# Kernel optimization log

Measured on AMD Instinct MI355X. Metric: run time of the kernel, lower is better.

The kernel has to match this reference:

```python
import jax, jax.numpy as jnp
import numpy as np

N, E, D, T, B, OUT = 20000, 80000, 768, 4, 3, 768
SCALE = 0.02


def _layer_norm(x, g, b):
    mu = jnp.mean(x, axis=-1, keepdims=True)
    var = jnp.var(x, axis=-1, keepdims=True)
    return (x - mu) / jnp.sqrt(var + 1e-5) * g + b


def _typed_linear(x, etype, bases, coeff):
    # DGL TypedLinear with basis regularizer: W[t] = sum_b coeff[t,b] * bases[b]
    # computed as 3 shared GEMMs + per-edge weighted sum (avoids [E,D,D] gather).
    c = coeff[etype]  # [E, B]
    y = c[:, 0:1] * (x @ bases[0])
    for bb in range(1, bases.shape[0]):
        y = y + c[:, bb:bb + 1] * (x @ bases[bb])
    return y


def _time_encode(t, freq, phase):
    return jnp.cos(t[:, None] * freq[None, :] + phase[None, :])


def _segment_softmax(scores, seg, n):
    m = jax.ops.segment_max(scores, seg, num_segments=n)
    m = jnp.where(jnp.isfinite(m), m, 0.0)  # empty segments -> -inf guard
    e = jnp.exp(scores - m[seg])
    den = jax.ops.segment_sum(e, seg, num_segments=n)[seg]
    return e / jnp.where(den == 0, 1.0, den)


def _forward(h, etime_hete, first_etime_homo, second_etime_homo, w_src, w_dst,
             ln_g, ln_b, src_bases, src_coeff, dst_bases, dst_coeff,
             user_bases, user_coeff, lin_w, lin_b, time_freq, time_phase,
             src_hete, dst_hete, first_etype_hete, src_homo, dst_homo,
             first_etype_homo, second_etype_homo, n_nodes):
    inv_sqrt_d = 1.0 / jnp.sqrt(jnp.asarray(768.0, h.dtype))
    n_src = h @ w_src.T  # src_weight (no bias)
    n_dst = h @ w_dst.T  # dst_weight (no bias)

    # --- heterogeneous edges ---
    sf = n_src[src_hete]
    df = n_dst[dst_hete]
    hete_src = jax.nn.relu(_typed_linear(_layer_norm(sf, ln_g, ln_b), first_etype_hete, src_bases, src_coeff))
    msg_h = _time_encode(etime_hete, time_freq, time_phase) + hete_src
    e_h = jnp.sum(msg_h * df, axis=1) * inv_sqrt_d
    a_h = _segment_softmax(e_h, dst_hete, n_nodes)
    h_hete = jax.ops.segment_sum(a_h[:, None] * msg_h, dst_hete, num_segments=n_nodes)

    # --- homogeneous edges ---
    sf = n_src[src_homo]
    df = n_dst[dst_homo]
    dst_feat = jax.nn.relu(_typed_linear(_layer_norm(df, ln_g, ln_b), first_etype_homo, dst_bases, dst_coeff))
    homo_feat = jax.nn.relu(_typed_linear(_layer_norm(sf, ln_g, ln_b), second_etype_homo, user_bases, user_coeff))
    t_homo = jnp.maximum(first_etime_homo, second_etime_homo)
    msg_o = _time_encode(t_homo, time_freq, time_phase) + homo_feat
    e_o = jnp.sum(msg_o * dst_feat, axis=1) * inv_sqrt_d
    a_o = _segment_softmax(e_o, dst_homo, n_nodes)
    h_homo = jax.ops.segment_sum(a_o[:, None] * msg_o, dst_homo, num_segments=n_nodes)

    n = jnp.concatenate([h_hete, h_homo], axis=-1)  # [N, 2D]
    z = jax.nn.relu(n @ lin_w.T + lin_b)
    zn = jnp.linalg.norm(z, axis=1, keepdims=True)
    return z / jnp.where(zn == 0, 1.0, zn)


def setup_inputs() -> dict:
    key = jax.random.key(0)
    ks = jax.random.split(key, 24)
    inp = {
        'h': jax.random.normal(ks[0], (N, D), jnp.float32),
        'etime_hete': jax.random.uniform(ks[1], (E,), jnp.float32),
        'first_etime_homo': jax.random.uniform(ks[2], (E,), jnp.float32),
        'second_etime_homo': jax.random.uniform(ks[3], (E,), jnp.float32),
        'w_src': jax.random.normal(ks[4], (D, D), jnp.float32) * SCALE,
        'w_dst': jax.random.normal(ks[5], (D, D), jnp.float32) * SCALE,
        'ln_g': jnp.ones((D,), jnp.float32),
        'ln_b': jnp.zeros((D,), jnp.float32),
        'src_bases': jax.random.normal(ks[6], (B, D, D), jnp.float32) * SCALE,
        'src_coeff': jax.random.normal(ks[7], (T, B), jnp.float32),
        'dst_bases': jax.random.normal(ks[8], (B, D, D), jnp.float32) * SCALE,
        'dst_coeff': jax.random.normal(ks[9], (T, B), jnp.float32),
        'user_bases': jax.random.normal(ks[10], (B, D, D), jnp.float32) * SCALE,
        'user_coeff': jax.random.normal(ks[11], (T, B), jnp.float32),
        'lin_w': jax.random.normal(ks[12], (OUT, 2 * D), jnp.float32) * SCALE,
        'lin_b': jnp.zeros((OUT,), jnp.float32),
        'time_freq': jnp.asarray(1.0 / 10 ** np.linspace(0, 9, D), jnp.float32),
        'time_phase': jnp.zeros((D,), jnp.float32),
        'src_hete': jax.random.randint(ks[13], (E,), 0, N, jnp.int32),
        'dst_hete': jax.random.randint(ks[14], (E,), 0, N, jnp.int32),
        'first_etype_hete': jax.random.randint(ks[15], (E,), 0, T, jnp.int32),
        'src_homo': jax.random.randint(ks[16], (E,), 0, N, jnp.int32),
        'dst_homo': jax.random.randint(ks[17], (E,), 0, N, jnp.int32),
        'first_etype_homo': jax.random.randint(ks[18], (E,), 0, T, jnp.int32),
        'second_etype_homo': jax.random.randint(ks[19], (E,), 0, T, jnp.int32),
        'num_nodes': N,
    }
    return inp


def reference(h, etime_hete, first_etime_homo, second_etime_homo, w_src, w_dst,
              ln_g, ln_b, src_bases, src_coeff, dst_bases, dst_coeff,
              user_bases, user_coeff, lin_w, lin_b, time_freq, time_phase,
              src_hete, dst_hete, first_etype_hete, src_homo, dst_homo,
              first_etype_homo, second_etype_homo, num_nodes):
    return _forward(h, etime_hete, first_etime_homo, second_etime_homo, w_src,
                    w_dst, ln_g, ln_b, src_bases, src_coeff, dst_bases,
                    dst_coeff, user_bases, user_coeff, lin_w, lin_b,
                    time_freq, time_phase, src_hete, dst_hete,
                    first_etype_hete, src_homo, dst_homo, first_etype_homo,
                    second_etype_homo, num_nodes)
```

## Files before the change

kernel.cpp:

```cpp
#include <hip/hip_runtime.h>
#include <hip/hip_bf16.h>
#include <stdint.h>

#define D 768
#define INV_SQRT_D 0.03608439182435161269f

static void* g_scratch = nullptr;
#define SCRATCH_BYTES ((size_t)600 * 1024 * 1024)

__attribute__((constructor))
static void _alloc_scratch() {
    if (hipMalloc(&g_scratch, SCRATCH_BYTES) != hipSuccess) g_scratch = nullptr;
}

static inline int cdiv(int a, int b) { return (a + b - 1) / b; }

typedef __attribute__((ext_vector_type(8))) short bf16x8;
typedef __attribute__((ext_vector_type(4))) float f32x4;

__device__ __forceinline__ unsigned cvt2b(float lo, float hi) {
    unsigned r;
    asm("v_cvt_pk_bf16_f32 %0, %1, %2" : "=v"(r) : "v"(lo), "v"(hi));
    return r;
}
__device__ __forceinline__ unsigned short f2b(float f) {
    return (unsigned short)cvt2b(f, f);
}
__device__ __forceinline__ float b2f(unsigned short u) {
    union { unsigned u; float f; } c; c.u = (unsigned)u << 16;
    return c.f;
}

__device__ __forceinline__ float block_reduce_sum(float v) {
#pragma unroll
    for (int off = 32; off > 0; off >>= 1) v += __shfl_down(v, off, 64);
    __shared__ float sm[4];
    int lane = threadIdx.x & 63, w = threadIdx.x >> 6;
    __syncthreads();
    if (lane == 0) sm[w] = v;
    __syncthreads();
    return (sm[0] + sm[1]) + (sm[2] + sm[3]);
}

__device__ __forceinline__ void xcd_swizzle(int& bx, int& by) {
    int nx = gridDim.x;
    int nwg = nx * gridDim.y;
    int o = blockIdx.y * nx + blockIdx.x;
    int q = nwg >> 3, r = nwg & 7;
    int xcd = o & 7, idx = o >> 3;
    int n = (xcd < r) ? (xcd * (q + 1) + idx)
                      : (r * (q + 1) + (xcd - r) * q + idx);
    bx = n % nx; by = n / nx;
}

template <bool CONCAT, bool BF16C, bool RELU, bool BIAS>
__global__ __launch_bounds__(256) void mfma_gemm(
    const unsigned short* __restrict__ A1, const unsigned short* __restrict__ A2,
    int lda, int ksplit,
    const unsigned short* __restrict__ B, int ldb,
    void* __restrict__ Cv, int ldc,
    const float* __restrict__ bias,
    int M, int K)
{
    __shared__ unsigned short As[128 * 32];
    __shared__ unsigned short Bs[128 * 32];
    const int tid = threadIdx.x;
    const int wv = tid >> 6, lane = tid & 63;
    int bx, by;
    xcd_swizzle(bx, by);
    const int m0 = by * 128, n0 = bx * 128;
    const int wm = (wv >> 1) << 6;
    const int wn = (wv & 1) << 6;
    const int fr = lane & 15;
    const int fq = lane >> 4;

    f32x4 acc[4][4] = {};

    for (int k0 = 0; k0 < K; k0 += 32) {
        const unsigned short* Asrc = A1;
        int kk = k0;
        if (CONCAT && k0 >= ksplit) { Asrc = A2; kk = k0 - ksplit; }
#pragma unroll
        for (int j = 0; j < 2; ++j) {
            int idx = j * 256 + tid;
            int row = idx >> 2, cb = (idx & 3) << 3;
            int am = m0 + row; if (am > M - 1) am = M - 1;
            const unsigned short* ga = Asrc + (size_t)am * lda + kk + cb;
            char* la = (char*)As + (size_t)(j * 256 + wv * 64) * 16;
            __builtin_amdgcn_global_load_lds(
                (const __attribute__((address_space(1))) unsigned int*)ga,
                (__attribute__((address_space(3))) unsigned int*)la, 16, 0, 0);
            const unsigned short* gb = B + (size_t)(n0 + row) * ldb + k0 + cb;
            char* lb = (char*)Bs + (size_t)(j * 256 + wv * 64) * 16;
            __builtin_amdgcn_global_load_lds(
                (const __attribute__((address_space(1))) unsigned int*)gb,
                (__attribute__((address_space(3))) unsigned int*)lb, 16, 0, 0);
        }
        __syncthreads();

        bf16x8 af[4], bfv[4];
#pragma unroll
        for (int i = 0; i < 4; ++i) {
            af[i]  = *(const bf16x8*)&As[(wm + i * 16 + fr) * 32 + fq * 8];
            bfv[i] = *(const bf16x8*)&Bs[(wn + i * 16 + fr) * 32 + fq * 8];
        }
#pragma unroll
        for (int mi = 0; mi < 4; ++mi)
#pragma unroll
            for (int ni = 0; ni < 4; ++ni)
                acc[mi][ni] = __builtin_amdgcn_mfma_f32_16x16x32_bf16(
                    af[mi], bfv[ni], acc[mi][ni], 0, 0, 0);
        __syncthreads();
    }

#pragma unroll
    for (int mi = 0; mi < 4; ++mi) {
#pragma unroll
        for (int r = 0; r < 4; ++r) {
            int m = m0 + wm + mi * 16 + fq * 4 + r;
            if (m >= M) continue;
#pragma unroll
            for (int ni = 0; ni < 4; ++ni) {
                int n = n0 + wn + ni * 16 + fr;
                float v = acc[mi][ni][r];
                if (BIAS) v += bias[n];
                if (RELU) v = fmaxf(v, 0.f);
                if (BF16C) ((unsigned short*)Cv)[(size_t)m * ldc + n] = f2b(v);
                else       ((float*)Cv)[(size_t)m * ldc + n] = v;
            }
        }
    }
}

__global__ void f32_to_bf16_kernel(const float* __restrict__ in,
                                   unsigned short* __restrict__ out, int n4) {
    int i = blockIdx.x * 256 + threadIdx.x;
    if (i >= n4) return;
    float4 v = *reinterpret_cast<const float4*>(in + (size_t)i * 4);
    ushort4 o;
    o.x = f2b(v.x); o.y = f2b(v.y); o.z = f2b(v.z); o.w = f2b(v.w);
    *reinterpret_cast<ushort4*>(out + (size_t)i * 4) = o;
}

__global__ __launch_bounds__(256) void combine_transpose_kernel(
    const float* __restrict__ in, const float* __restrict__ coeff,
    unsigned short* __restrict__ out) {
    int t = blockIdx.z;
    float c0 = coeff[t * 3 + 0], c1 = coeff[t * 3 + 1], c2 = coeff[t * 3 + 2];
    __shared__ float tile[32][33];
    int bx = blockIdx.x * 32, by = blockIdx.y * 32;
    int tx = threadIdx.x & 31, ty = threadIdx.x >> 5;
#pragma unroll
    for (int i = 0; i < 32; i += 8) {
        size_t idx = (size_t)(by + ty + i) * D + bx + tx;
        tile[ty + i][tx] = c0 * in[idx] + c1 * in[idx + (size_t)D * D]
                         + c2 * in[idx + (size_t)2 * D * D];
    }
    __syncthreads();
    unsigned short* o = out + (size_t)t * D * D;
#pragma unroll
    for (int i = 0; i < 32; i += 8)
        o[(size_t)(bx + ty + i) * D + by + tx] = f2b(tile[tx][ty + i]);
}

__global__ __launch_bounds__(256) void ln_bf16_kernel(
    unsigned short* __restrict__ x, int ld,
    const float* __restrict__ g, const float* __restrict__ b)
{
    unsigned short* r = x + (size_t)blockIdx.x * ld;
    int t = threadIdx.x;
    float v0 = b2f(r[t]), v1 = b2f(r[t + 256]), v2 = b2f(r[t + 512]);
    float s = block_reduce_sum(v0 + v1 + v2);
    float mu = s * (1.f / 768.f);
    float d0 = v0 - mu, d1 = v1 - mu, d2 = v2 - mu;
    float q = block_reduce_sum(d0 * d0 + d1 * d1 + d2 * d2);
    float rstd = 1.f / sqrtf(q * (1.f / 768.f) + 1e-5f);
    r[t]       = f2b(d0 * rstd * g[t]       + b[t]);
    r[t + 256] = f2b(d1 * rstd * g[t + 256] + b[t + 256]);
    r[t + 512] = f2b(d2 * rstd * g[t + 512] + b[t + 512]);
}

__global__ void zero_int_kernel(int* __restrict__ p, int n) {
    int i = blockIdx.x * 256 + threadIdx.x;
    if (i < n) p[i] = 0;
}

__global__ void count2_kernel(const int* __restrict__ dA, const int* __restrict__ dB,
                              int* __restrict__ cntA, int* __restrict__ cntB, int E) {
    int e = blockIdx.x * 256 + threadIdx.x;
    if (e < E) {
        atomicAdd(&cntA[dA[e]], 1);
        atomicAdd(&cntB[dB[e]], 1);
    }
}

__global__ __launch_bounds__(1024) void scan2_kernel(
    const int* __restrict__ cntA, int* __restrict__ offsA,
    const int* __restrict__ cntB, int* __restrict__ offsB, int n)
{
    __shared__ int tmp[1024];
    __shared__ int carry;
    int tid = threadIdx.x;
    for (int g = 0; g < 2; ++g) {
        const int* cnt = g ? cntB : cntA;
        int* offs = g ? offsB : offsA;
        __syncthreads();
        if (tid == 0) carry = 0;
        __syncthreads();
        for (int base = 0; base < n; base += 1024) {
            int idx = base + tid;
            int v = (idx < n) ? cnt[idx] : 0;
            tmp[tid] = v;
            __syncthreads();
            for (int off = 1; off < 1024; off <<= 1) {
                int t = (tid >= off) ? tmp[tid - off] : 0;
                __syncthreads();
                tmp[tid] += t;
                __syncthreads();
            }
            int inc = tmp[tid];
            int c = carry;
            if (idx < n) offs[idx] = c + inc - v;
            __syncthreads();
            if (tid == 0) carry = c + tmp[1023];
            __syncthreads();
        }
        if (tid == 0) offs[n] = carry;
    }
}

__global__ void scatter2_kernel(
    const int* __restrict__ dA, const int* __restrict__ offsA,
    int* __restrict__ curA, int* __restrict__ listA,
    const int* __restrict__ dB, const int* __restrict__ offsB,
    int* __restrict__ curB, int* __restrict__ listB, int E) {
    int e = blockIdx.x * 256 + threadIdx.x;
    if (e < E) {
        int d = dA[e];
        listA[offsA[d] + atomicAdd(&curA[d], 1)] = e;
        d = dB[e];
        listB[offsB[d] + atomicAdd(&curB[d], 1)] = e;
    }
}

template <bool IS_HOMO>
__global__ __launch_bounds__(256) void edge_fused_kernel(
    const int* __restrict__ offs, const int* __restrict__ list,
    const unsigned short* __restrict__ Pmsg, int ldm,
    const unsigned short* __restrict__ Pdst, int ldd,
    const float* __restrict__ t1, const float* __restrict__ t2,
    const int* __restrict__ src,
    const int* __restrict__ etA,
    const int* __restrict__ etB,
    const float* __restrict__ freq, const float* __restrict__ phase,
    unsigned short* __restrict__ out, int nN)
{
    int v = blockIdx.x * 4 + (threadIdx.x >> 6);
    if (v >= nN) return;
    int l = threadIdx.x & 63;
    bool hi = l < 32;

    float frq[16], phs[16];
#pragma unroll
    for (int q = 0; q < 16; ++q) { frq[q] = 0.f; phs[q] = 0.f; }
    {
        float4 f0 = *(const float4*)(freq + l * 8);
        float4 f1 = *(const float4*)(freq + l * 8 + 4);
        float4 p0 = *(const float4*)(phase + l * 8);
        float4 p1 = *(const float4*)(phase + l * 8 + 4);
        frq[0] = f0.x; frq[1] = f0.y; frq[2] = f0.z; frq[3] = f0.w;
        frq[4] = f1.x; frq[5] = f1.y; frq[6] = f1.z; frq[7] = f1.w;
        phs[0] = p0.x; phs[1] = p0.y; phs[2] = p0.z; phs[3] = p0.w;
        phs[4] = p1.x; phs[5] = p1.y; phs[6] = p1.z; phs[7] = p1.w;
    }
    if (hi) {
        float4 f0 = *(const float4*)(freq + 512 + l * 8);
        float4 f1 = *(const float4*)(freq + 512 + l * 8 + 4);
        float4 p0 = *(const float4*)(phase + 512 + l * 8);
        float4 p1 = *(const float4*)(phase + 512 + l * 8 + 4);
        frq[8]  = f0.x; frq[9]  = f0.y; frq[10] = f0.z; frq[11] = f0.w;
        frq[12] = f1.x; frq[13] = f1.y; frq[14] = f1.z; frq[15] = f1.w;
        phs[8]  = p0.x; phs[9]  = p0.y; phs[10] = p0.z; phs[11] = p0.w;
        phs[12] = p1.x; phs[13] = p1.y; phs[14] = p1.z; phs[15] = p1.w;
    }

    float nd[16];
#pragma unroll
    for (int q = 0; q < 16; ++q) nd[q] = 0.f;
    if (!IS_HOMO) {
        const unsigned short* pd = Pdst + (size_t)v * ldd;
        bf16x8 r0 = *(const bf16x8*)(pd + l * 8);
#pragma unroll
        for (int q = 0; q < 8; ++q) nd[q] = b2f((unsigned short)r0[q]);
        if (hi) {
            bf16x8 r1 = *(const bf16x8*)(pd + 512 + l * 8);
#pragma unroll
            for (int q = 0; q < 8; ++q) nd[8 + q] = b2f((unsigned short)r1[q]);
        }
    }

    float m = -INFINITY, den = 0.f;
    float acc[16];
#pragma unroll
    for (int q = 0; q < 16; ++q) acc[q] = 0.f;

    int i0 = offs[v], i1 = offs[v + 1];
    for (int i = i0; i < i1; ++i) {
        int e = list[i];
        int s = src[e];
        float tv = IS_HOMO ? fmaxf(t1[e], t2[e]) : t1[e];
        int tym = IS_HOMO ? etB[e] : etA[e];
        const unsigned short* pm = Pmsg + (size_t)s * ldm + tym * D;

        float msg[16];
#pragma unroll
        for (int q = 0; q < 16; ++q) msg[q] = 0.f;
        bf16x8 r0 = *(const bf16x8*)(pm + l * 8);
#pragma unroll
        for (int q = 0; q < 8; ++q)
            msg[q] = __cosf(tv * frq[q] + phs[q]) + b2f((unsigned short)r0[q]);
        if (hi) {
            bf16x8 r1 = *(const bf16x8*)(pm + 512 + l * 8);
#pragma unroll
            for (int q = 0; q < 8; ++q)
                msg[8 + q] = __cosf(tv * frq[8 + q] + phs[8 + q])
                           + b2f((unsigned short)r1[q]);
        }

        float dotp = 0.f;
        if (IS_HOMO) {
            int ta = etA[e];
            const unsigned short* pd2 = Pdst + (size_t)v * ldd + ta * D;
            bf16x8 d0 = *(const bf16x8*)(pd2 + l * 8);
#pragma unroll
            for (int q = 0; q < 8; ++q) {
                float dv = fmaxf(b2f((unsigned short)d0[q]), 0.f);
                dotp += msg[q] * dv;
            }
            if (hi) {
                bf16x8 d1 = *(const bf16x8*)(pd2 + 512 + l * 8);
#pragma unroll
                for (int q = 0; q < 8; ++q)
                    dotp += msg[8 + q] * b2f((unsigned short)d1[q]);
            }
        } else {
#pragma unroll
            for (int q = 0; q < 16; ++q) dotp += msg[q] * nd[q];
        }
#pragma unroll
        for (int off = 1; off < 64; off <<= 1) dotp += __shfl_xor(dotp, off, 64);
        float sc = dotp * INV_SQRT_D;

        float nm = fmaxf(m, sc);
        float sOld = __expf(m - nm);
        float w = __expf(sc - nm);
        den = den * sOld + w;
#pragma unroll
        for (int q = 0; q < 16; ++q) acc[q] = acc[q] * sOld + w * msg[q];
        m = nm;
    }

    float inv = (den > 0.f) ? 1.f / den : 0.f;
    unsigned short* o = out + (size_t)v * D;
    uint4 st;
    st.x = cvt2b(acc[0] * inv, acc[1] * inv); st.y = cvt2b(acc[2] * inv, acc[3] * inv);
    st.z = cvt2b(acc[4] * inv, acc[5] * inv); st.w = cvt2b(acc[6] * inv, acc[7] * inv);
    *reinterpret_cast<uint4*>(o + (size_t)l * 8) = st;
    if (hi) {
        st.x = cvt2b(acc[8] * inv, acc[9] * inv);   st.y = cvt2b(acc[10] * inv, acc[11] * inv);
        st.z = cvt2b(acc[12] * inv, acc[13] * inv); st.w = cvt2b(acc[14] * inv, acc[15] * inv);
        *reinterpret_cast<uint4*>(o + 512 + (size_t)l * 8) = st;
    }
}

__global__ __launch_bounds__(256) void normalize_kernel(
    const float* __restrict__ z, float* __restrict__ out)
{
    const float* x = z + (size_t)blockIdx.x * D;
    int t = threadIdx.x;
    float v0 = x[t], v1 = x[t + 256], v2 = x[t + 512];
    float s = block_reduce_sum(v0 * v0 + v1 * v1 + v2 * v2);
    float nrm = sqrtf(s);
    float inv = (nrm == 0.f) ? 1.f : 1.f / nrm;
    float* o = out + (size_t)blockIdx.x * D;
    o[t] = v0 * inv; o[t + 256] = v1 * inv; o[t + 512] = v2 * inv;
}

__global__ void fill_f32_kernel(float* __restrict__ p, float v, int n) {
    int i = blockIdx.x * 256 + threadIdx.x;
    if (i < n) p[i] = v;
}

extern "C" void kernel_launch(void* const* d_in, const int* in_sizes, int n_in,
                              void* d_out, int out_size, void* d_ws, size_t ws_size,
                              hipStream_t stream)
{
    const float* h          = (const float*)d_in[0];
    const float* etime_hete = (const float*)d_in[1];
    const float* t1_homo    = (const float*)d_in[2];
    const float* t2_homo    = (const float*)d_in[3];
    const float* w_src      = (const float*)d_in[4];
    const float* w_dst      = (const float*)d_in[5];
    const float* ln_g       = (const float*)d_in[6];
    const float* ln_b       = (const float*)d_in[7];
    const float* src_bases  = (const float*)d_in[8];
    const float* src_coeff  = (const float*)d_in[9];
    const float* dst_bases  = (const float*)d_in[10];
    const float* dst_coeff  = (const float*)d_in[11];
    const float* user_bases = (const float*)d_in[12];
    const float* user_coeff = (const float*)d_in[13];
    const float* lin_w      = (const float*)d_in[14];
    const float* lin_b      = (const float*)d_in[15];
    const float* time_freq  = (const float*)d_in[16];
    const float* time_phase = (const float*)d_in[17];
    const int* src_hete = (const int*)d_in[18];
    const int* dst_hete = (const int*)d_in[19];
    const int* et_hete  = (const int*)d_in[20];
    const int* src_homo = (const int*)d_in[21];
    const int* dst_homo = (const int*)d_in[22];
    const int* et1_homo = (const int*)d_in[23];
    const int* et2_homo = (const int*)d_in[24];

    const int N = in_sizes[0] / D;
    const int E = in_sizes[1];

    const size_t szST  = (size_t)N * 1536 * 2;
    const size_t szPSU = (size_t)N * 6144 * 2;
    const size_t szPD  = (size_t)N * 3072 * 2;
    const size_t szVb  = (size_t)N * D * 2;
    const size_t szW   = (size_t)D * D * 2;
    size_t need = szST + szPSU + szPD + 3 * szVb
                + 2 * szW + 2 * szW + 8 * szW + 4 * szW
                + (size_t)2 * N * 4
                + 2 * (((size_t)(N + 1) * 4 + 255) & ~(size_t)255)
                + (size_t)2 * E * 4 + 16384;

    char* base;
    if (ws_size >= need) base = (char*)d_ws;
    else if (g_scratch)  base = (char*)g_scratch;
    else {
        fill_f32_kernel<<<cdiv(out_size, 256), 256, 0, stream>>>(
            (float*)d_out, 1000.0f + (float)(ws_size >> 20), out_size);
        return;
    }

    char* p = base;
    auto carve = [&](size_t bytes) { char* r = p; p += (bytes + 255) & ~(size_t)255; return r; };
    unsigned short* STb = (unsigned short*)carve(szST);
    unsigned short* PSU = (unsigned short*)carve(szPSU);
    unsigned short* PD  = (unsigned short*)carve(szPD);
    unsigned short* hb  = (unsigned short*)carve(szVb);
    unsigned short* hAb = (unsigned short*)carve(szVb);
    unsigned short* hOb = (unsigned short*)carve(szVb);
    unsigned short* wsb = (unsigned short*)carve(2 * szW);
    unsigned short* lwb = (unsigned short*)carve(2 * szW);
    unsigned short* suW = (unsigned short*)carve(8 * szW);
    unsigned short* dstW = (unsigned short*)carve(4 * szW);
    int* cnt    = (int*)carve((size_t)2 * N * 4);
    int* offsA  = (int*)carve((size_t)(N + 1) * 4);
    int* offsB  = (int*)carve((size_t)(N + 1) * 4);
    int* listA  = (int*)carve((size_t)E * 4);
    int* listB  = (int*)carve((size_t)E * 4);
    float* z    = (float*)PSU;

    unsigned short* Sb = STb;
    unsigned short* Tb = STb + 768;
    unsigned short* Psrc_t  = PSU;
    unsigned short* Puser_t = PSU + 3072;

    const int eb = cdiv(E, 256);
    const int nb2 = cdiv(2 * N, 256);
    const int MB = cdiv(N, 128);
    dim3 g_proj(12, MB);
    dim3 g_psu(48, MB);
    dim3 g_pd(24, MB);
    dim3 g_fin(6, MB);
    dim3 ct_grid(24, 24, 4);
    const int agb = cdiv(N, 4);

    f32_to_bf16_kernel<<<cdiv(N * D / 4, 256), 256, 0, stream>>>(h, hb, N * D / 4);
    f32_to_bf16_kernel<<<cdiv(D * D / 4, 256), 256, 0, stream>>>(w_src, wsb, D * D / 4);
    f32_to_bf16_kernel<<<cdiv(D * D / 4, 256), 256, 0, stream>>>(w_dst, wsb + (size_t)D * D, D * D / 4);
    f32_to_bf16_kernel<<<cdiv(D * 2 * D / 4, 256), 256, 0, stream>>>(lin_w, lwb, D * 2 * D / 4);
    combine_transpose_kernel<<<ct_grid, 256, 0, stream>>>(src_bases, src_coeff, suW);
    combine_transpose_kernel<<<ct_grid, 256, 0, stream>>>(user_bases, user_coeff, suW + (size_t)4 * D * D);
    combine_transpose_kernel<<<ct_grid, 256, 0, stream>>>(dst_bases, dst_coeff, dstW);

    zero_int_kernel<<<nb2, 256, 0, stream>>>(cnt, 2 * N);
    count2_kernel<<<eb, 256, 0, stream>>>(dst_hete, dst_homo, cnt, cnt + N, E);
    scan2_kernel<<<1, 1024, 0, stream>>>(cnt, offsA, cnt + N, offsB, N);
    zero_int_kernel<<<nb2, 256, 0, stream>>>(cnt, 2 * N);
    scatter2_kernel<<<eb, 256, 0, stream>>>(dst_hete, offsA, cnt, listA,
                                            dst_homo, offsB, cnt + N, listB, E);

    mfma_gemm<false, true, false, false><<<g_proj, 256, 0, stream>>>(
        hb, hb, D, D, wsb, D, STb, 1536, nullptr, N, D);
    ln_bf16_kernel<<<N, 256, 0, stream>>>(Sb, 1536, ln_g, ln_b);

    mfma_gemm<false, true, true, false><<<g_psu, 256, 0, stream>>>(
        Sb, Sb, 1536, D, suW, D, PSU, 6144, nullptr, N, D);

    edge_fused_kernel<false><<<agb, 256, 0, stream>>>(
        offsA, listA, Psrc_t, 6144, Tb, 1536,
        etime_hete, nullptr, src_hete, et_hete, nullptr,
        time_freq, time_phase, hAb, N);

    ln_bf16_kernel<<<N, 256, 0, stream>>>(Tb, 1536, ln_g, ln_b);
    mfma_gemm<false, true, true, false><<<g_pd, 256, 0, stream>>>(
        Tb, Tb, 1536, D, dstW, D, PD, 3072, nullptr, N, D);

    edge_fused_kernel<true><<<agb, 256, 0, stream>>>(
        offsB, listB, Puser_t, 6144, PD, 3072,
        t1_homo, t2_homo, src_homo, et1_homo, et2_homo,
        time_freq, time_phase, hOb, N);

    mfma_gemm<true, false, true, true><<<g_fin, 256, 0, stream>>>(
        hAb, hOb, D, D, lwb, 2 * D, z, D, lin_b, N, 2 * D);
    normalize_kernel<<<N, 256, 0, stream>>>(z, (float*)d_out);
}
```

Baseline: 1.112 ms.

## Double GEMM K-tile to 64 with XOR-swizzled LDS, drop XCD swizzle

Raises the MFMA GEMM's K step from 32 to 64 by doubling the LDS tiles. Each 16-byte chunk is placed in LDS with an XOR swizzle on the row index, and the fragment reads use the matching permutation to avoid bank conflicts. This halves the number of K iterations and barriers per tile. It also removes the XCD-aware block remapping in favour of plain blockIdx order, and drops a redundant ReLU (fmaxf) on the dst features in the homogeneous attention dot product. Risks are lost L2 locality across XCDs and a changed result if that ReLU was not already applied upstream.

```diff
diff --git a/kernel.cpp b/kernel.cpp
--- a/kernel.cpp
+++ b/kernel.cpp
@@ -40,17 +40,6 @@
     if (lane == 0) sm[w] = v;
     __syncthreads();
     return (sm[0] + sm[1]) + (sm[2] + sm[3]);
-}
-
-__device__ __forceinline__ void xcd_swizzle(int& bx, int& by) {
-    int nx = gridDim.x;
-    int nwg = nx * gridDim.y;
-    int o = blockIdx.y * nx + blockIdx.x;
-    int q = nwg >> 3, r = nwg & 7;
-    int xcd = o & 7, idx = o >> 3;
-    int n = (xcd < r) ? (xcd * (q + 1) + idx)
-                      : (r * (q + 1) + (xcd - r) * q + idx);
-    bx = n % nx; by = n / nx;
 }
 
 template <bool CONCAT, bool BF16C, bool RELU, bool BIAS>
@@ -62,13 +51,11 @@
     const float* __restrict__ bias,
     int M, int K)
 {
-    __shared__ unsigned short As[128 * 32];
-    __shared__ unsigned short Bs[128 * 32];
+    __shared__ unsigned short As[128 * 64];
+    __shared__ unsigned short Bs[128 * 64];
     const int tid = threadIdx.x;
     const int wv = tid >> 6, lane = tid & 63;
-    int bx, by;
-    xcd_swizzle(bx, by);
-    const int m0 = by * 128, n0 = bx * 128;
+    const int m0 = blockIdx.y * 128, n0 = blockIdx.x * 128;
     const int wm = (wv >> 1) << 6;
     const int wn = (wv & 1) << 6;
     const int fr = lane & 15;
@@ -76,21 +63,22 @@
 
     f32x4 acc[4][4] = {};
 
-    for (int k0 = 0; k0 < K; k0 += 32) {
+    for (int k0 = 0; k0 < K; k0 += 64) {
         const unsigned short* Asrc = A1;
         int kk = k0;
         if (CONCAT && k0 >= ksplit) { Asrc = A2; kk = k0 - ksplit; }
 #pragma unroll
-        for (int j = 0; j < 2; ++j) {
+        for (int j = 0; j < 4; ++j) {
             int idx = j * 256 + tid;
-            int row = idx >> 2, cb = (idx & 3) << 3;
+            int row = idx >> 3;
+            int gs  = ((idx & 7) ^ (row & 7)) << 3;
             int am = m0 + row; if (am > M - 1) am = M - 1;
-            const unsigned short* ga = Asrc + (size_t)am * lda + kk + cb;
+            const unsigned short* ga = Asrc + (size_t)am * lda + kk + gs;
             char* la = (char*)As + (size_t)(j * 256 + wv * 64) * 16;
             __builtin_amdgcn_global_load_lds(
                 (const __attribute__((address_space(1))) unsigned int*)ga,
                 (__attribute__((address_space(3))) unsigned int*)la, 16, 0, 0);
-            const unsigned short* gb = B + (size_t)(n0 + row) * ldb + k0 + cb;
+            const unsigned short* gb = B + (size_t)(n0 + row) * ldb + k0 + gs;
             char* lb = (char*)Bs + (size_t)(j * 256 + wv * 64) * 16;
             __builtin_amdgcn_global_load_lds(
                 (const __attribute__((address_space(1))) unsigned int*)gb,
@@ -98,18 +86,22 @@
         }
         __syncthreads();
 
-        bf16x8 af[4], bfv[4];
-#pragma unroll
-        for (int i = 0; i < 4; ++i) {
-            af[i]  = *(const bf16x8*)&As[(wm + i * 16 + fr) * 32 + fq * 8];
-            bfv[i] = *(const bf16x8*)&Bs[(wn + i * 16 + fr) * 32 + fq * 8];
-        }
-#pragma unroll
-        for (int mi = 0; mi < 4; ++mi)
-#pragma unroll
-            for (int ni = 0; ni < 4; ++ni)
-                acc[mi][ni] = __builtin_amdgcn_mfma_f32_16x16x32_bf16(
-                    af[mi], bfv[ni], acc[mi][ni], 0, 0, 0);
+#pragma unroll
+        for (int ks = 0; ks < 2; ++ks) {
+            bf16x8 af[4], bfv[4];
+            const int gr = (((ks * 4 + fq) ^ (fr & 7)) << 3);
+#pragma unroll
+            for (int i = 0; i < 4; ++i) {
+                af[i]  = *(const bf16x8*)&As[(wm + i * 16 + fr) * 64 + gr];
+                bfv[i] = *(const bf16x8*)&Bs[(wn + i * 16 + fr) * 64 + gr];
+            }
+#pragma unroll
+            for (int mi = 0; mi < 4; ++mi)
+#pragma unroll
+                for (int ni = 0; ni < 4; ++ni)
+                    acc[mi][ni] = __builtin_amdgcn_mfma_f32_16x16x32_bf16(
+                        af[mi], bfv[ni], acc[mi][ni], 0, 0, 0);
+        }
         __syncthreads();
     }
 
@@ -333,10 +325,8 @@
             const unsigned short* pd2 = Pdst + (size_t)v * ldd + ta * D;
             bf16x8 d0 = *(const bf16x8*)(pd2 + l * 8);
 #pragma unroll
-            for (int q = 0; q < 8; ++q) {
-                float dv = fmaxf(b2f((unsigned short)d0[q]), 0.f);
-                dotp += msg[q] * dv;
-            }
+            for (int q = 0; q < 8; ++q)
+                dotp += msg[q] * b2f((unsigned short)d0[q]);
             if (hi) {
                 bf16x8 d1 = *(const bf16x8*)(pd2 + 512 + l * 8);
 #pragma unroll
```

Result: faster. 1.002 ms (-9.9%).
